# Optimization experiments

Hardware: AMD Instinct MI355X
Metric: run time of the kernel (lower is better)

## Reference

```python
import jax, jax.numpy as jnp
import numpy as np
import math

D_MODEL = 512
NHEAD = 8
HEAD_DIM = D_MODEL // NHEAD
MAX_REL = 128
B, T, S = 4, 2048, 2048


def setup_inputs() -> dict:
    key = jax.random.key(0)
    ks = jax.random.split(key, 16)
    sc = 1.0 / math.sqrt(D_MODEL)
    inp = {
        "query": jax.random.normal(ks[0], (B, T, D_MODEL), jnp.float32),
        "key": jax.random.normal(ks[1], (B, S, D_MODEL), jnp.float32),
        "value": jax.random.normal(ks[2], (B, S, D_MODEL), jnp.float32),
        "Wq": jax.random.normal(ks[3], (D_MODEL, D_MODEL), jnp.float32) * sc,
        "bq": jnp.zeros((D_MODEL,), jnp.float32),
        "Wk": jax.random.normal(ks[4], (D_MODEL, D_MODEL), jnp.float32) * sc,
        "bk": jnp.zeros((D_MODEL,), jnp.float32),
        "Wv": jax.random.normal(ks[5], (D_MODEL, D_MODEL), jnp.float32) * sc,
        "bv": jnp.zeros((D_MODEL,), jnp.float32),
        "Wo": jax.random.normal(ks[6], (D_MODEL, D_MODEL), jnp.float32) * sc,
        "bo": jnp.zeros((D_MODEL,), jnp.float32),
        "rel_emb": jax.random.normal(ks[7], (2 * MAX_REL + 1, NHEAD), jnp.float32) * 0.02,
    }
    return inp


def reference(query, key, value, Wq, bq, Wk, bk, Wv, bv, Wo, bo, rel_emb):
    # linear projections (torch Linear: x @ W.T + b), split heads -> [B,H,T,Dh]
    def proj(x, W, b, L):
        return (x @ W.T + b).reshape(B, L, NHEAD, HEAD_DIM).transpose(0, 2, 1, 3)

    q = proj(query, Wq, bq, T)
    k = proj(key, Wk, bk, S)
    v = proj(value, Wv, bv, S)

    scores = jnp.einsum("bhtd,bhsd->bhts", q, k) / math.sqrt(HEAD_DIM)

    # relative position bias lookup: rel[t,s] = clamp(t-s) + max_rel -> [H,T,S]
    rel = jnp.arange(T)[:, None] - jnp.arange(S)[None, :]
    rel = jnp.clip(rel, -MAX_REL, MAX_REL) + MAX_REL
    bias = rel_emb[rel].transpose(2, 0, 1)  # [H,T,S]
    scores = scores + bias[None]

    w = jax.nn.softmax(scores, axis=-1)  # dropout p used in eval mode -> identity
    out = jnp.einsum("bhts,bhsd->bhtd", w, v)
    out = out.transpose(0, 2, 1, 3).reshape(B, T, D_MODEL)
    return out @ Wo.T + bo
```

## Files before the change

kernel.cpp:

```cpp
#include <hip/hip_runtime.h>

typedef __attribute__((ext_vector_type(4))) float f32x4;
typedef __attribute__((ext_vector_type(16))) float f32x16;
typedef __attribute__((ext_vector_type(4))) unsigned short u16x4;
typedef __attribute__((ext_vector_type(8))) unsigned short u16x8;
typedef __attribute__((ext_vector_type(4))) unsigned int u32x4;
typedef __attribute__((ext_vector_type(8))) __bf16 bf16x8;

#define SZX_E ((size_t)4 * 2048 * 512)
#define SZW_E ((size_t)512 * 512)

__device__ __forceinline__ unsigned short f2bf(float f) {
  unsigned int u = __builtin_bit_cast(unsigned int, f);
  u += 0x7fffu + ((u >> 16) & 1u);
  return (unsigned short)(u >> 16);
}

__device__ __forceinline__ bf16x8 ld_bf8(const unsigned short* p) {
  return __builtin_bit_cast(bf16x8, *(const u16x8*)p);
}

__device__ __forceinline__ f32x4 mfma16(bf16x8 a, bf16x8 b, f32x4 c) {
  return __builtin_amdgcn_mfma_f32_16x16x32_bf16(a, b, c, 0, 0, 0);
}

__device__ __forceinline__ f32x16 mfma32(bf16x8 a, bf16x8 b, f32x16 c) {
  return __builtin_amdgcn_mfma_f32_32x32x16_bf16(a, b, c, 0, 0, 0);
}

__device__ __forceinline__ unsigned int cvt_pk_bf16(float lo, float hi) {
  unsigned int r;
  asm("v_cvt_pk_bf16_f32 %0, %1, %2" : "=v"(r) : "v"(lo), "v"(hi));
  return r;
}

__device__ __forceinline__ void plane32_swap(unsigned int& a, unsigned int& b) {
  asm("v_permlane32_swap_b32 %0, %1" : "+v"(a), "+v"(b));
}

__device__ __forceinline__ float exp2_fast(float x) {
  float r;
  asm("v_exp_f32 %0, %1" : "=v"(r) : "v"(x));
  return r;
}

__device__ __forceinline__ void gload16(const void* g, void* l) {
  __builtin_amdgcn_global_load_lds(
      (const __attribute__((address_space(1))) unsigned int*)g,
      (__attribute__((address_space(3))) unsigned int*)l, 16, 0, 0);
}

__global__ __launch_bounds__(256) void cvt_all(const float* __restrict__ q_,
                                               const float* __restrict__ k_,
                                               const float* __restrict__ v_,
                                               const float* __restrict__ wq_,
                                               const float* __restrict__ wk_,
                                               const float* __restrict__ wv_,
                                               const float* __restrict__ wo_,
                                               unsigned short* __restrict__ out) {
  const int bq = blockIdx.x;
  const float* src;
  size_t segbase, li;
  if (bq < 12288) {
    const int s = bq >> 12;
    src = (s == 0) ? q_ : (s == 1) ? k_ : v_;
    li = (size_t)(bq & 4095) * 256 + threadIdx.x;
    segbase = (size_t)s * 4194304;
  } else {
    const int s = (bq - 12288) >> 8;
    src = (s == 0) ? wq_ : (s == 1) ? wk_ : (s == 2) ? wv_ : wo_;
    li = (size_t)((bq - 12288) & 255) * 256 + threadIdx.x;
    segbase = 12582912 + (size_t)s * 262144;
  }
  const f32x4 v = *(const f32x4*)(src + li * 4);
  u16x4 r;
  r[0] = f2bf(v[0]); r[1] = f2bf(v[1]); r[2] = f2bf(v[2]); r[3] = f2bf(v[3]);
  *(u16x4*)(out + segbase + li * 4) = r;
}

__global__ __launch_bounds__(256) void gemm_qkv(const unsigned short* __restrict__ base,
                                                const float* __restrict__ bq,
                                                const float* __restrict__ bk,
                                                const float* __restrict__ bv,
                                                unsigned short* __restrict__ outb) {
  __shared__ unsigned short Asb[2][4096];
  __shared__ unsigned short Bsb[2][4096];
  const int z = blockIdx.z;
  const unsigned short* A = base + (size_t)z * SZX_E;
  const unsigned short* Bw = base + 3 * SZX_E + (size_t)z * SZW_E;
  const float* bias = (z == 0) ? bq : (z == 1) ? bk : bv;

  const int tid = threadIdx.x;
  const int l = tid & 63;
  const int w = tid >> 6;
  const int g = l >> 4;
  const int lr = l & 15;
  const int mB = blockIdx.y * 128;
  const int nB = blockIdx.x * 128;
  const int m0 = (w >> 1) * 64;
  const int n0 = (w & 1) * 64;
  const int ubase = tid & ~63;

  auto stage = [&](int bufi, int kk) {
#pragma unroll
    for (int i = 0; i < 2; i++) {
      const int idx = i * 256 + tid;
      const int ub = i * 256 + ubase;
      const int r = idx >> 2, c = idx & 3;
      gload16((const char*)A + ((size_t)(mB + r) * 512 + kk + c * 8) * 2,
              (char*)&Asb[bufi][0] + ub * 16);
      gload16((const char*)Bw + ((size_t)(nB + r) * 512 + kk + c * 8) * 2,
              (char*)&Bsb[bufi][0] + ub * 16);
    }
  };

  f32x4 acc[4][4];
#pragma unroll
  for (int i = 0; i < 4; i++)
#pragma unroll
    for (int j = 0; j < 4; j++) acc[i][j] = f32x4{0.f, 0.f, 0.f, 0.f};

  stage(0, 0);
  __syncthreads();
  int buf = 0;

  for (int ks = 0; ks < 16; ++ks) {
    if (ks < 15) stage(buf ^ 1, (ks + 1) * 32);
    bf16x8 af[4], bfr[4];
#pragma unroll
    for (int t = 0; t < 4; t++) {
      af[t] = ld_bf8(&Asb[buf][(m0 + t * 16 + lr) * 32 + g * 8]);
      bfr[t] = ld_bf8(&Bsb[buf][(n0 + t * 16 + lr) * 32 + g * 8]);
    }
#pragma unroll
    for (int i = 0; i < 4; i++)
#pragma unroll
      for (int j = 0; j < 4; j++)
        acc[i][j] = mfma16(af[i], bfr[j], acc[i][j]);
    __syncthreads();
    buf ^= 1;
  }

  unsigned short* outz = outb + (size_t)z * SZX_E;
#pragma unroll
  for (int j = 0; j < 4; j++) {
    const int n = nB + n0 + j * 16 + lr;
    const float bn = bias[n];
#pragma unroll
    for (int i = 0; i < 4; i++) {
#pragma unroll
      for (int r = 0; r < 4; r++) {
        const int m = mB + m0 + i * 16 + g * 4 + r;
        const float v = acc[i][j][r] + bn;
        if (z < 2) {
          outz[(size_t)m * 512 + n] = f2bf(v);
        } else {
          const int bb = m >> 11, s = m & 2047;
          const int hh = n >> 6, d = n & 63;
          outz[((size_t)((bb * 8 + hh) * 64 + d) << 11) + s] = f2bf(v);
        }
      }
    }
  }
}

__global__ __launch_bounds__(256) void gemm_o(const unsigned short* __restrict__ A,
                                              const unsigned short* __restrict__ Bw,
                                              const float* __restrict__ bias,
                                              float* __restrict__ Cout) {
  __shared__ unsigned short Asb[2][4096];
  __shared__ unsigned short Bsb[2][4096];
  const int tid = threadIdx.x;
  const int l = tid & 63;
  const int w = tid >> 6;
  const int g = l >> 4;
  const int lr = l & 15;
  const int mB = blockIdx.y * 128;
  const int nB = blockIdx.x * 128;
  const int m0 = (w >> 1) * 64;
  const int n0 = (w & 1) * 64;
  const int ubase = tid & ~63;

  auto stage = [&](int bufi, int kk) {
#pragma unroll
    for (int i = 0; i < 2; i++) {
      const int idx = i * 256 + tid;
      const int ub = i * 256 + ubase;
      const int r = idx >> 2, c = idx & 3;
      gload16((const char*)A + ((size_t)(mB + r) * 512 + kk + c * 8) * 2,
              (char*)&Asb[bufi][0] + ub * 16);
      gload16((const char*)Bw + ((size_t)(nB + r) * 512 + kk + c * 8) * 2,
              (char*)&Bsb[bufi][0] + ub * 16);
    }
  };

  f32x4 acc[4][4];
#pragma unroll
  for (int i = 0; i < 4; i++)
#pragma unroll
    for (int j = 0; j < 4; j++) acc[i][j] = f32x4{0.f, 0.f, 0.f, 0.f};

  stage(0, 0);
  __syncthreads();
  int buf = 0;

  for (int ks = 0; ks < 16; ++ks) {
    if (ks < 15) stage(buf ^ 1, (ks + 1) * 32);
    bf16x8 af[4], bfr[4];
#pragma unroll
    for (int t = 0; t < 4; t++) {
      af[t] = ld_bf8(&Asb[buf][(m0 + t * 16 + lr) * 32 + g * 8]);
      bfr[t] = ld_bf8(&Bsb[buf][(n0 + t * 16 + lr) * 32 + g * 8]);
    }
#pragma unroll
    for (int i = 0; i < 4; i++)
#pragma unroll
      for (int j = 0; j < 4; j++)
        acc[i][j] = mfma16(af[i], bfr[j], acc[i][j]);
    __syncthreads();
    buf ^= 1;
  }

#pragma unroll
  for (int j = 0; j < 4; j++) {
    const int n = nB + n0 + j * 16 + lr;
    const float bn = bias[n];
#pragma unroll
    for (int i = 0; i < 4; i++) {
#pragma unroll
      for (int r = 0; r < 4; r++) {
        const int m = mB + m0 + i * 16 + g * 4 + r;
        Cout[(size_t)m * 512 + n] = acc[i][j][r] + bn;
      }
    }
  }
}

__global__ __launch_bounds__(256, 2) void attn_kernel(const unsigned short* __restrict__ Qp,
                                                      const unsigned short* __restrict__ Kp,
                                                      const unsigned short* __restrict__ Vt,
                                                      const float* __restrict__ rel_emb,
                                                      unsigned short* __restrict__ At) {
  __shared__ float bias_s[257];
  __shared__ unsigned short K_lds[2][4096];
  __shared__ unsigned short V_lds[2][4096];
  const int bid0 = blockIdx.x;
  const int lg = (bid0 & 7) * 64 + (bid0 >> 3);
  const int qb = lg & 15;
  const int h = (lg >> 4) & 7;
  const int b = lg >> 7;
  const int tid = threadIdx.x;
  const int lane = tid & 63, w = tid >> 6;
  const int hi = lane >> 5, q31 = lane & 31;
  const int q0w = qb * 128 + w * 32;
  const int tq = q0w + q31;
  const float SCL = 0.125f * 1.44269504f;

  const char* kstage = (const char*)Kp + ((size_t)b * 2048 * 512 + h * 64) * 2;
  const char* vstage = (const char*)Vt + ((size_t)(b * 8 + h) * 64 * 2048) * 2;

  auto stage = [&](int bufi, int s0n) {
#pragma unroll
    for (int ii = 0; ii < 4; ii++) {
      const int ins = (w & 1) * 4 + ii;
      const int rr = ins * 8 + (lane >> 3);
      const int ch = (lane & 7) ^ (rr & 7);
      if (w < 2) {
        gload16(kstage + (size_t)(s0n + rr) * 1024 + ch * 16,
                (char*)&K_lds[bufi][0] + ins * 1024);
      } else {
        gload16(vstage + (size_t)rr * 4096 + (size_t)s0n * 2 + ch * 16,
                (char*)&V_lds[bufi][0] + ins * 1024);
      }
    }
  };

  for (int i = tid; i < 257; i += 256) bias_s[i] = rel_emb[i * 8 + h] * 1.44269504f;
  stage(0, 0);
  __syncthreads();
  const float bias_lo = bias_s[0], bias_hi = bias_s[256];

  const unsigned short* qptr = Qp + (size_t)(b * 2048 + tq) * 512 + h * 64 + hi * 8;
  const bf16x8 qf0 = ld_bf8(qptr);
  const bf16x8 qf1 = ld_bf8(qptr + 16);
  const bf16x8 qf2 = ld_bf8(qptr + 32);
  const bf16x8 qf3 = ld_bf8(qptr + 48);

  const f32x16 z16 = {0.f, 0.f, 0.f, 0.f, 0.f, 0.f, 0.f, 0.f,
                      0.f, 0.f, 0.f, 0.f, 0.f, 0.f, 0.f, 0.f};
  f32x16 o_lo = z16, o_hi = z16;
  float l_run = 0.f;
  int buf = 0;

  for (int t = 0; t < 32; ++t) {
    const int s0 = t * 64;
    if (t != 31) stage(buf ^ 1, s0 + 64);

    const unsigned short* kb = &K_lds[buf][0];
    const int rswz = q31 & 7;
    f32x16 sa, sb;
    sa = mfma32(ld_bf8(kb + q31 * 64 + (((0 + hi) ^ rswz) << 3)), qf0, z16);
    sb = mfma32(ld_bf8(kb + (32 + q31) * 64 + (((0 + hi) ^ rswz) << 3)), qf0, z16);
    sa = mfma32(ld_bf8(kb + q31 * 64 + (((2 + hi) ^ rswz) << 3)), qf1, sa);
    sb = mfma32(ld_bf8(kb + (32 + q31) * 64 + (((2 + hi) ^ rswz) << 3)), qf1, sb);
    sa = mfma32(ld_bf8(kb + q31 * 64 + (((4 + hi) ^ rswz) << 3)), qf2, sa);
    sb = mfma32(ld_bf8(kb + (32 + q31) * 64 + (((4 + hi) ^ rswz) << 3)), qf2, sb);
    sa = mfma32(ld_bf8(kb + q31 * 64 + (((6 + hi) ^ rswz) << 3)), qf3, sa);
    sb = mfma32(ld_bf8(kb + (32 + q31) * 64 + (((6 + hi) ^ rswz) << 3)), qf3, sb);

    const unsigned short* vb = &V_lds[buf][0];
    bf16x8 vl[4], vh[4];
#pragma unroll
    for (int ks = 0; ks < 4; ks++) {
      vl[ks] = ld_bf8(vb + q31 * 64 + (((ks * 2 + hi) ^ rswz) << 3));
      vh[ks] = ld_bf8(vb + (32 + q31) * 64 + (((ks * 2 + hi) ^ rswz) << 3));
    }

    const int relmin = q0w - s0 - 63;
    const int relmax = q0w + 31 - s0;
    float SCL2, off0;
    if (relmin >= 128 || relmax <= -128) {
      SCL2 = SCL;
      off0 = (relmin >= 128) ? bias_hi : bias_lo;
    } else {
#pragma unroll
      for (int r = 0; r < 16; r++) {
        const int rowA = (r & 3) + 8 * (r >> 2) + 4 * hi;
        const int rA = tq - s0 - rowA;
        const int rB = rA - 32;
        const int iA = (rA < -128 ? -128 : (rA > 128 ? 128 : rA)) + 128;
        const int iB = (rB < -128 ? -128 : (rB > 128 ? 128 : rB)) + 128;
        sa[r] = fmaf(sa[r], SCL, bias_s[iA]);
        sb[r] = fmaf(sb[r], SCL, bias_s[iB]);
      }
      SCL2 = 1.f;
      off0 = 0.f;
    }

#pragma unroll
    for (int r = 0; r < 16; r++) {
      sa[r] = exp2_fast(fmaf(sa[r], SCL2, off0));
      sb[r] = exp2_fast(fmaf(sb[r], SCL2, off0));
    }
    float s8[8];
#pragma unroll
    for (int i = 0; i < 8; i++)
      s8[i] = (sa[i] + sa[i + 8]) + (sb[i] + sb[i + 8]);
    float ps = ((s8[0] + s8[1]) + (s8[2] + s8[3])) + ((s8[4] + s8[5]) + (s8[6] + s8[7]));
    ps += __shfl_xor(ps, 32, 64);
    l_run += ps;

    bf16x8 pa[4];
#pragma unroll
    for (int ks = 0; ks < 4; ks++) {
      const int c8 = (ks & 1) * 8;
      const f32x16& src = (ks < 2) ? sa : sb;
      unsigned int a0 = cvt_pk_bf16(src[c8 + 0], src[c8 + 1]);
      unsigned int b0 = cvt_pk_bf16(src[c8 + 4], src[c8 + 5]);
      unsigned int a1 = cvt_pk_bf16(src[c8 + 2], src[c8 + 3]);
      unsigned int b1 = cvt_pk_bf16(src[c8 + 6], src[c8 + 7]);
      plane32_swap(a0, b0);
      plane32_swap(a1, b1);
      pa[ks] = __builtin_bit_cast(bf16x8, u32x4{a0, a1, b0, b1});
    }

#pragma unroll
    for (int ks = 0; ks < 4; ks++) {
      o_lo = mfma32(pa[ks], vl[ks], o_lo);
      o_hi = mfma32(pa[ks], vh[ks], o_hi);
    }

    __syncthreads();
    buf ^= 1;
  }

  const float inv = 1.f / l_run;
#pragma unroll
  for (int r2 = 0; r2 < 16; r2++) {
    const int ro = (r2 & 3) + 8 * (r2 >> 2) + 4 * hi;
    const float rr = __shfl(inv, ro, 64);
    unsigned short* op = At + (size_t)(b * 2048 + q0w + ro) * 512 + h * 64;
    op[q31] = f2bf(o_lo[r2] * rr);
    op[32 + q31] = f2bf(o_hi[r2] * rr);
  }
}

extern "C" void kernel_launch(void* const* d_in, const int* in_sizes, int n_in,
                              void* d_out, int out_size, void* d_ws, size_t ws_size,
                              hipStream_t stream) {
  const float* query = (const float*)d_in[0];
  const float* key   = (const float*)d_in[1];
  const float* value = (const float*)d_in[2];
  const float* Wq = (const float*)d_in[3];
  const float* bq = (const float*)d_in[4];
  const float* Wk = (const float*)d_in[5];
  const float* bk = (const float*)d_in[6];
  const float* Wv = (const float*)d_in[7];
  const float* bv = (const float*)d_in[8];
  const float* Wo = (const float*)d_in[9];
  const float* bo = (const float*)d_in[10];
  const float* rel = (const float*)d_in[11];

  char* ws = (char*)d_ws;
  unsigned short* base = (unsigned short*)ws;
  unsigned short* wo = base + 3 * SZX_E + 3 * SZW_E;
  unsigned short* Qp = base + 3 * SZX_E + 4 * SZW_E;
  unsigned short* Kp = Qp + SZX_E;
  unsigned short* Vt = Kp + SZX_E;
  unsigned short* At = Vt + SZX_E;

  cvt_all<<<dim3(13312), dim3(256), 0, stream>>>(query, key, value, Wq, Wk, Wv, Wo, base);

  dim3 blk(256);
  gemm_qkv<<<dim3(4, 64, 3), blk, 0, stream>>>(base, bq, bk, bv, Qp);

  attn_kernel<<<dim3(512), blk, 0, stream>>>(Qp, Kp, Vt, rel, At);

  gemm_o<<<dim3(4, 64), blk, 0, stream>>>(At, wo, bo, (float*)d_out);
}
```

Before: 107.4 us.

## Split each KV tile across warp pairs in attention and merge partial outputs

```diff
diff --git a/kernel.cpp b/kernel.cpp
--- a/kernel.cpp
+++ b/kernel.cpp
@@ -236,7 +236,7 @@
   }
 }
 
-__global__ __launch_bounds__(256, 2) void attn_kernel(const unsigned short* __restrict__ Qp,
+__global__ __launch_bounds__(256, 4) void attn_kernel(const unsigned short* __restrict__ Qp,
                                                       const unsigned short* __restrict__ Kp,
                                                       const unsigned short* __restrict__ Vt,
                                                       const float* __restrict__ rel_emb,
@@ -245,14 +245,15 @@
   __shared__ unsigned short K_lds[2][4096];
   __shared__ unsigned short V_lds[2][4096];
   const int bid0 = blockIdx.x;
-  const int lg = (bid0 & 7) * 64 + (bid0 >> 3);
-  const int qb = lg & 15;
-  const int h = (lg >> 4) & 7;
-  const int b = lg >> 7;
+  const int lg = (bid0 & 7) * 128 + (bid0 >> 3);
+  const int qb = lg & 31;
+  const int h = (lg >> 5) & 7;
+  const int b = lg >> 8;
   const int tid = threadIdx.x;
   const int lane = tid & 63, w = tid >> 6;
+  const int qg = w >> 1, kh = w & 1;
   const int hi = lane >> 5, q31 = lane & 31;
-  const int q0w = qb * 128 + w * 32;
+  const int q0w = qb * 64 + qg * 32;
   const int tq = q0w + q31;
   const float SCL = 0.125f * 1.44269504f;
 
@@ -261,17 +262,14 @@
 
   auto stage = [&](int bufi, int s0n) {
 #pragma unroll
-    for (int ii = 0; ii < 4; ii++) {
-      const int ins = (w & 1) * 4 + ii;
+    for (int ii = 0; ii < 2; ii++) {
+      const int ins = w * 2 + ii;
       const int rr = ins * 8 + (lane >> 3);
       const int ch = (lane & 7) ^ (rr & 7);
-      if (w < 2) {
-        gload16(kstage + (size_t)(s0n + rr) * 1024 + ch * 16,
-                (char*)&K_lds[bufi][0] + ins * 1024);
-      } else {
-        gload16(vstage + (size_t)rr * 4096 + (size_t)s0n * 2 + ch * 16,
-                (char*)&V_lds[bufi][0] + ins * 1024);
-      }
+      gload16(kstage + (size_t)(s0n + rr) * 1024 + ch * 16,
+              (char*)&K_lds[bufi][0] + ins * 1024);
+      gload16(vstage + (size_t)rr * 4096 + (size_t)s0n * 2 + ch * 16,
+              (char*)&V_lds[bufi][0] + ins * 1024);
     }
   };
 
@@ -291,30 +289,28 @@
   f32x16 o_lo = z16, o_hi = z16;
   float l_run = 0.f;
   int buf = 0;
+  const int kvb = kh * 32;
+  const int rswz = q31 & 7;
 
   for (int t = 0; t < 32; ++t) {
     const int s0 = t * 64;
     if (t != 31) stage(buf ^ 1, s0 + 64);
 
     const unsigned short* kb = &K_lds[buf][0];
-    const int rswz = q31 & 7;
-    f32x16 sa, sb;
-    sa = mfma32(ld_bf8(kb + q31 * 64 + (((0 + hi) ^ rswz) << 3)), qf0, z16);
-    sb = mfma32(ld_bf8(kb + (32 + q31) * 64 + (((0 + hi) ^ rswz) << 3)), qf0, z16);
-    sa = mfma32(ld_bf8(kb + q31 * 64 + (((2 + hi) ^ rswz) << 3)), qf1, sa);
-    sb = mfma32(ld_bf8(kb + (32 + q31) * 64 + (((2 + hi) ^ rswz) << 3)), qf1, sb);
-    sa = mfma32(ld_bf8(kb + q31 * 64 + (((4 + hi) ^ rswz) << 3)), qf2, sa);
-    sb = mfma32(ld_bf8(kb + (32 + q31) * 64 + (((4 + hi) ^ rswz) << 3)), qf2, sb);
-    sa = mfma32(ld_bf8(kb + q31 * 64 + (((6 + hi) ^ rswz) << 3)), qf3, sa);
-    sb = mfma32(ld_bf8(kb + (32 + q31) * 64 + (((6 + hi) ^ rswz) << 3)), qf3, sb);
+    f32x16 sa;
+    sa = mfma32(ld_bf8(kb + (kvb + q31) * 64 + (((0 + hi) ^ rswz) << 3)), qf0, z16);
+    sa = mfma32(ld_bf8(kb + (kvb + q31) * 64 + (((2 + hi) ^ rswz) << 3)), qf1, sa);
+    sa = mfma32(ld_bf8(kb + (kvb + q31) * 64 + (((4 + hi) ^ rswz) << 3)), qf2, sa);
+    sa = mfma32(ld_bf8(kb + (kvb + q31) * 64 + (((6 + hi) ^ rswz) << 3)), qf3, sa);
 
     const unsigned short* vb = &V_lds[buf][0];
-    bf16x8 vl[4], vh[4];
-#pragma unroll
-    for (int ks = 0; ks < 4; ks++) {
-      vl[ks] = ld_bf8(vb + q31 * 64 + (((ks * 2 + hi) ^ rswz) << 3));
-      vh[ks] = ld_bf8(vb + (32 + q31) * 64 + (((ks * 2 + hi) ^ rswz) << 3));
-    }
+    bf16x8 vf[2][2];
+#pragma unroll
+    for (int oh = 0; oh < 2; oh++)
+#pragma unroll
+      for (int kc = 0; kc < 2; kc++)
+        vf[oh][kc] = ld_bf8(vb + (oh * 32 + q31) * 64 +
+                            (((kh * 4 + kc * 2 + hi) ^ rswz) << 3));
 
     const int relmin = q0w - s0 - 63;
     const int relmax = q0w + 31 - s0;
@@ -326,62 +322,70 @@
 #pragma unroll
       for (int r = 0; r < 16; r++) {
         const int rowA = (r & 3) + 8 * (r >> 2) + 4 * hi;
-        const int rA = tq - s0 - rowA;
-        const int rB = rA - 32;
+        const int rA = tq - (s0 + kvb) - rowA;
         const int iA = (rA < -128 ? -128 : (rA > 128 ? 128 : rA)) + 128;
-        const int iB = (rB < -128 ? -128 : (rB > 128 ? 128 : rB)) + 128;
         sa[r] = fmaf(sa[r], SCL, bias_s[iA]);
-        sb[r] = fmaf(sb[r], SCL, bias_s[iB]);
       }
       SCL2 = 1.f;
       off0 = 0.f;
     }
 
 #pragma unroll
-    for (int r = 0; r < 16; r++) {
-      sa[r] = exp2_fast(fmaf(sa[r], SCL2, off0));
-      sb[r] = exp2_fast(fmaf(sb[r], SCL2, off0));
-    }
-    float s8[8];
-#pragma unroll
-    for (int i = 0; i < 8; i++)
-      s8[i] = (sa[i] + sa[i + 8]) + (sb[i] + sb[i + 8]);
-    float ps = ((s8[0] + s8[1]) + (s8[2] + s8[3])) + ((s8[4] + s8[5]) + (s8[6] + s8[7]));
+    for (int r = 0; r < 16; r++) sa[r] = exp2_fast(fmaf(sa[r], SCL2, off0));
+    float s4[4];
+#pragma unroll
+    for (int i = 0; i < 4; i++)
+      s4[i] = (sa[i] + sa[i + 4]) + (sa[i + 8] + sa[i + 12]);
+    float ps = (s4[0] + s4[1]) + (s4[2] + s4[3]);
     ps += __shfl_xor(ps, 32, 64);
     l_run += ps;
 
-    bf16x8 pa[4];
-#pragma unroll
-    for (int ks = 0; ks < 4; ks++) {
-      const int c8 = (ks & 1) * 8;
-      const f32x16& src = (ks < 2) ? sa : sb;
-      unsigned int a0 = cvt_pk_bf16(src[c8 + 0], src[c8 + 1]);
-      unsigned int b0 = cvt_pk_bf16(src[c8 + 4], src[c8 + 5]);
-      unsigned int a1 = cvt_pk_bf16(src[c8 + 2], src[c8 + 3]);
-      unsigned int b1 = cvt_pk_bf16(src[c8 + 6], src[c8 + 7]);
+    bf16x8 pa[2];
+#pragma unroll
+    for (int kc = 0; kc < 2; kc++) {
+      const int c8 = kc * 8;
+      unsigned int a0 = cvt_pk_bf16(sa[c8 + 0], sa[c8 + 1]);
+      unsigned int b0 = cvt_pk_bf16(sa[c8 + 4], sa[c8 + 5]);
+      unsigned int a1 = cvt_pk_bf16(sa[c8 + 2], sa[c8 + 3]);
+      unsigned int b1 = cvt_pk_bf16(sa[c8 + 6], sa[c8 + 7]);
       plane32_swap(a0, b0);
       plane32_swap(a1, b1);
-      pa[ks] = __builtin_bit_cast(bf16x8, u32x4{a0, a1, b0, b1});
-    }
-
-#pragma unroll
-    for (int ks = 0; ks < 4; ks++) {
-      o_lo = mfma32(pa[ks], vl[ks], o_lo);
-      o_hi = mfma32(pa[ks], vh[ks], o_hi);
-    }
+      pa[kc] = __builtin_bit_cast(bf16x8, u32x4{a0, a1, b0, b1});
+    }
+
+    o_lo = mfma32(pa[0], vf[0][0], o_lo);
+    o_hi = mfma32(pa[0], vf[1][0], o_hi);
+    o_lo = mfma32(pa[1], vf[0][1], o_lo);
+    o_hi = mfma32(pa[1], vf[1][1], o_hi);
 
     __syncthreads();
     buf ^= 1;
   }
 
-  const float inv = 1.f / l_run;
-#pragma unroll
-  for (int r2 = 0; r2 < 16; r2++) {
-    const int ro = (r2 & 3) + 8 * (r2 >> 2) + 4 * hi;
-    const float rr = __shfl(inv, ro, 64);
-    unsigned short* op = At + (size_t)(b * 2048 + q0w + ro) * 512 + h * 64;
-    op[q31] = f2bf(o_lo[r2] * rr);
-    op[32 + q31] = f2bf(o_hi[r2] * rr);
+  float* o_comb = (float*)&K_lds[0][0];
+  float* l_comb = (float*)&V_lds[0][0];
+  if (kh == 1) {
+#pragma unroll
+    for (int r2 = 0; r2 < 16; r2++) {
+      const int ro = (r2 & 3) + 8 * (r2 >> 2) + 4 * hi;
+      o_comb[(qg * 32 + ro) * 64 + q31] = o_lo[r2];
+      o_comb[(qg * 32 + ro) * 64 + 32 + q31] = o_hi[r2];
+    }
+    if (hi == 0) l_comb[qg * 32 + q31] = l_run;
+  }
+  __syncthreads();
+  if (kh == 0) {
+#pragma unroll
+    for (int r2 = 0; r2 < 16; r2++) {
+      const int ro = (r2 & 3) + 8 * (r2 >> 2) + 4 * hi;
+      const float lsum = __shfl(l_run, ro, 64) + l_comb[qg * 32 + ro];
+      const float rr = 1.f / lsum;
+      const float v_lo = o_lo[r2] + o_comb[(qg * 32 + ro) * 64 + q31];
+      const float v_hi = o_hi[r2] + o_comb[(qg * 32 + ro) * 64 + 32 + q31];
+      unsigned short* op = At + (size_t)(b * 2048 + q0w + ro) * 512 + h * 64;
+      op[q31] = f2bf(v_lo * rr);
+      op[32 + q31] = f2bf(v_hi * rr);
+    }
   }
 }
 
@@ -414,7 +418,7 @@
   dim3 blk(256);
   gemm_qkv<<<dim3(4, 64, 3), blk, 0, stream>>>(base, bq, bk, bv, Qp);
 
-  attn_kernel<<<dim3(512), blk, 0, stream>>>(Qp, Kp, Vt, rel, At);
+  attn_kernel<<<dim3(1024), blk, 0, stream>>>(Qp, Kp, Vt, rel, At);
 
   gemm_o<<<dim3(4, 64), blk, 0, stream>>>(At, wo, bo, (float*)d_out);
 }
```

Measured after the change: 116.0 us. 8.0% more time.
